# Kernel tuning notes

Measured on AMD Instinct MI355X. Metric: run time of the kernel, lower is better.

The kernel has to match this reference:

```python
import jax, jax.numpy as jnp
import numpy as np

B, S, H, C, T = 8, 1024, 256, 4, 12
THETA = 10000.0


def setup_inputs() -> dict:
    key = jax.random.key(0)
    ks = jax.random.split(key, 7)
    x = jax.random.normal(ks[0], (B, S, H), dtype=jnp.float32)
    token_index = jax.random.randint(ks[1], (B, S), 0, 256, dtype=jnp.int32)
    thread_id = jnp.sort(jax.random.randint(ks[2], (B, S), 0, T, dtype=jnp.int32), axis=-1)
    bound = 1.0 / np.sqrt(H)  # nn.Linear default init range
    Wq = jax.random.uniform(ks[3], (H, H * C), jnp.float32, -bound, bound)
    bq = jax.random.uniform(ks[4], (H * C,), jnp.float32, -bound, bound)
    Wk = jax.random.uniform(ks[5], (H, H * C), jnp.float32, -bound, bound)
    bk = jax.random.uniform(ks[6], (H * C,), jnp.float32, -bound, bound)
    return {"x": x, "Wq": Wq, "bq": bq, "Wk": Wk, "bk": bk,
            "token_index": token_index, "thread_id": thread_id}


def _rope(v, pos):
    # v: (B, S, C, H); pos: (B, S) signed positions
    half = v.shape[-1] // 2
    # freqs = 1 / theta^(arange(0, H, 2) / H)
    freqs = 1.0 / (THETA ** (jnp.arange(half, dtype=jnp.float32) * 2.0 / (2 * half)))
    ang = pos[..., None].astype(jnp.float32) * freqs          # (B, S, half)
    cos = jnp.cos(ang)[:, :, None, :]                          # (B, S, 1, half)
    sin = jnp.sin(ang)[:, :, None, :]
    vr = v.reshape(*v.shape[:-1], half, 2)                     # complex pairs (even, odd)
    re = vr[..., 0] * cos - vr[..., 1] * sin
    im = vr[..., 0] * sin + vr[..., 1] * cos
    return jnp.stack([re, im], axis=-1).reshape(v.shape)


def reference(x, Wq, bq, Wk, bk, token_index, thread_id):
    q = (x @ Wq + bq).reshape(B, S, C, H)
    k = (x @ Wk + bk).reshape(B, S, C, H)
    # Block sign rules of get_instance_embedding reduce to three cases per
    # token pair (m, n) with thread ids ti=thread(m), tj=thread(n):
    #   0 < ti < tj : q uses -pos, k uses +pos
    #   0 < tj < ti : q uses +pos, k uses -pos
    #   otherwise   : both use +pos
    q_pos = _rope(q, token_index)
    q_neg = _rope(q, -token_index)
    k_pos = _rope(k, token_index)
    k_neg = _rope(k, -token_index)
    l1 = jnp.einsum('bmch,bnch->bcmn', q_pos, k_pos)
    l2 = jnp.einsum('bmch,bnch->bcmn', q_neg, k_pos)
    l3 = jnp.einsum('bmch,bnch->bcmn', q_pos, k_neg)
    ti = thread_id[:, :, None]   # rows
    tj = thread_id[:, None, :]   # cols
    cond2 = ((ti > 0) & (ti < tj))[:, None, :, :]   # (B,1,S,S)
    cond3 = ((tj > 0) & (ti > tj))[:, None, :, :]
    return jnp.where(cond2, l2, jnp.where(cond3, l3, l1))  # (B, C, S, S)
```

## Files before the change

kernel.cpp:

```cpp
#include <hip/hip_runtime.h>

#define BB 8
#define SS 1024
#define HH 256
#define CC 4
#define NQ 1024

typedef unsigned short u16;
typedef unsigned int u32;
typedef __attribute__((ext_vector_type(8))) __bf16 bf16x8;
typedef __attribute__((ext_vector_type(4))) float f32x4;
typedef __attribute__((ext_vector_type(4))) u32 u32x4;
typedef __attribute__((ext_vector_type(4))) u16 u16x4;

__device__ __forceinline__ u16 f2bf(float f) {
    u32 u = __float_as_uint(f);
    u32 r = (u + 0x7FFFu + ((u >> 16) & 1u)) >> 16;
    return (u16)r;
}

__device__ __forceinline__ void gld16(const u16* g, u16* l) {
    __builtin_amdgcn_global_load_lds(
        (const __attribute__((address_space(1))) void*)g,
        (__attribute__((address_space(3))) void*)l, 16, 0, 0);
}

__device__ __forceinline__ bf16x8 ldsfrag(const u16* smem, int row, int c16) {
    const char* p = (const char*)smem + row * 128 + (((c16 ^ (row & 7)) & 7) << 4);
    return *(const bf16x8*)p;
}

__global__ void k0_castx(const float4* __restrict__ x, u16x4* __restrict__ xbf) {
    int i = blockIdx.x * 256 + threadIdx.x;
    float4 v = x[i];
    u16x4 o = {f2bf(v.x), f2bf(v.y), f2bf(v.z), f2bf(v.w)};
    xbf[i] = o;
}

__global__ void k0_transw(const float* __restrict__ Wq, const float* __restrict__ Wk,
                          u16* __restrict__ Wt) {
    __shared__ u16 tl[64][65];
    int nb = blockIdx.x * 64, kb = blockIdx.y * 64;
    int c = threadIdx.x & 63;
#pragma unroll
    for (int r = threadIdx.x >> 6; r < 64; r += 4) {
        int k = kb + r, n = nb + c;
        float v = (n < NQ) ? Wq[k * NQ + n] : Wk[k * NQ + (n - NQ)];
        tl[c][r] = f2bf(v);
    }
    __syncthreads();
#pragma unroll
    for (int r = threadIdx.x >> 6; r < 64; r += 4) {
        Wt[(size_t)(nb + r) * HH + kb + c] = tl[r][c];
    }
}

__global__ void k0_trig(float2* __restrict__ trig) {
    int i = blockIdx.x * 256 + threadIdx.x;
    int pos = i >> 7, f = i & 127;
    float freq = __expf(-(float)f * 0.07195578515529633f);
    float ang = (float)pos * freq;
    float s, c;
    sincosf(ang, &s, &c);
    trig[i] = make_float2(c, s);
}

#define STAGE_A(dst, srcbase, row0cnt4, m_off, kc)                                  \
    _Pragma("unroll") for (int i_ = 0; i_ < (row0cnt4); ++i_) {                     \
        int r_ = w * 8 * (row0cnt4) + i_ * 8 + (l >> 3);                            \
        int c16_ = (l & 7) ^ (r_ & 7);                                              \
        gld16((srcbase) + (size_t)((m_off) + r_) * HH + (kc) * 64 + c16_ * 8,       \
              (dst) + (w * 8 * (row0cnt4) + i_ * 8) * 64);                          \
    }

__global__ void __launch_bounds__(256) k1_proj(
    const u16* __restrict__ xbf, const u16* __restrict__ Wt,
    const float* __restrict__ bq, const float* __restrict__ bk,
    const int* __restrict__ tok, const float2* __restrict__ trig,
    u16* __restrict__ qpos, u16* __restrict__ qneg,
    u16* __restrict__ kpos, u16* __restrict__ kneg) {
    int wg = blockIdx.x;
    int m0 = (wg >> 5) * 128, n0 = (wg & 31) * 64;
    int w = threadIdx.x >> 6, l = threadIdx.x & 63;

    __shared__ u16 sm[24576];
    u16* Ab[2] = {sm, sm + 12288};
    u16* Bb[2] = {sm + 8192, sm + 20480};

    f32x4 acc[2][4] = {};
    STAGE_A(Ab[0], xbf, 4, m0, 0)
    STAGE_A(Bb[0], Wt, 2, n0, 0)
    asm volatile("s_waitcnt vmcnt(0)" ::: "memory");
    __builtin_amdgcn_s_barrier();
#pragma unroll
    for (int kc = 0; kc < 4; ++kc) {
        u16* As = Ab[kc & 1];
        u16* Bs = Bb[kc & 1];
        if (kc < 3) {
            STAGE_A(Ab[(kc + 1) & 1], xbf, 4, m0, kc + 1)
            STAGE_A(Bb[(kc + 1) & 1], Wt, 2, n0, kc + 1)
        }
#pragma unroll
        for (int ks = 0; ks < 2; ++ks) {
            int c16 = (l >> 4) + ks * 4;
            bf16x8 af[2], bfr[4];
#pragma unroll
            for (int mi = 0; mi < 2; ++mi) af[mi] = ldsfrag(As, w * 32 + mi * 16 + (l & 15), c16);
#pragma unroll
            for (int ns = 0; ns < 4; ++ns) bfr[ns] = ldsfrag(Bs, ns * 16 + (l & 15), c16);
#pragma unroll
            for (int mi = 0; mi < 2; ++mi)
#pragma unroll
                for (int ns = 0; ns < 4; ++ns)
                    acc[mi][ns] = __builtin_amdgcn_mfma_f32_16x16x32_bf16(af[mi], bfr[ns], acc[mi][ns], 0, 0, 0);
        }
        if (kc < 3) {
            asm volatile("s_waitcnt vmcnt(0) lgkmcnt(0)" ::: "memory");
            __builtin_amdgcn_s_barrier();
        }
    }

#pragma unroll
    for (int mi = 0; mi < 2; ++mi)
#pragma unroll
        for (int ns = 0; ns < 4; ++ns) {
            int n = n0 + ns * 16 + (l & 15);
            bool isq = n < NQ;
            int nc = n & (NQ - 1);
            float bias = isq ? bq[nc] : bk[nc];
            int c = nc >> 8, h = nc & 255, fi = h >> 1;
#pragma unroll
            for (int r = 0; r < 4; ++r) {
                int m = m0 + w * 32 + mi * 16 + (l >> 4) * 4 + r;
                float val = acc[mi][ns][r] + bias;
                float other = __shfl_xor(val, 1);
                int pos = tok[m];
                float2 cs = trig[pos * 128 + fi];
                float rp, rn;
                if ((l & 1) == 0) {
                    rp = val * cs.x - other * cs.y;
                    rn = val * cs.x + other * cs.y;
                } else {
                    rp = other * cs.y + val * cs.x;
                    rn = -other * cs.y + val * cs.x;
                }
                int b = m >> 10, s = m & 1023;
                size_t oidx = ((size_t)((b << 2) | c) * SS + s) * HH + h;
                if (isq) {
                    qpos[oidx] = f2bf(rp);
                    qneg[oidx] = f2bf(rn);
                } else {
                    kpos[oidx] = f2bf(rp);
                    kneg[oidx] = f2bf(rn);
                }
            }
        }
}

__global__ void __launch_bounds__(256) k2_gemm(
    const u16* __restrict__ qpos, const u16* __restrict__ qneg,
    const u16* __restrict__ kpos, const u16* __restrict__ kneg,
    const int* __restrict__ thread_id, float* __restrict__ out) {
    int wg = blockIdx.x;
    int bc = wg >> 7;
    int t = wg & 127;
    int m0 = (t >> 4) * 128, n0 = (t & 15) * 64;
    const int* tb = thread_id + (bc >> 2) * SS;
    int w = threadIdx.x >> 6, l = threadIdx.x & 63;
    int ti0 = tb[m0], ti1 = tb[m0 + 127], tj0 = tb[n0], tj1 = tb[n0 + 63];
    bool pure2 = (ti0 > 0) & (ti1 < tj0);
    bool pure3 = (tj0 > 0) & (ti0 > tj1);
    bool pure1 = (ti1 == 0) | (tj1 == 0) | ((ti0 == ti1) & (tj0 == tj1) & (ti0 == tj0));
    size_t base = (size_t)bc * (SS * HH);
    float* ob = out + (size_t)bc * ((size_t)SS * SS);
    int ar0 = m0 + w * 32;

    __shared__ u16 sm[24576];

    if (pure1 | pure2 | pure3) {
        const u16* q = (pure2 ? qneg : qpos) + base;
        const u16* k = (pure3 ? kneg : kpos) + base;
        u16* Ab[2] = {sm, sm + 12288};
        u16* Bb[2] = {sm + 8192, sm + 20480};

        f32x4 acc[2][4] = {};
        STAGE_A(Ab[0], q, 4, m0, 0)
        STAGE_A(Bb[0], k, 2, n0, 0)
        asm volatile("s_waitcnt vmcnt(0)" ::: "memory");
        __builtin_amdgcn_s_barrier();
#pragma unroll
        for (int kc = 0; kc < 4; ++kc) {
            u16* As = Ab[kc & 1];
            u16* Bs = Bb[kc & 1];
            if (kc < 3) {
                STAGE_A(Ab[(kc + 1) & 1], q, 4, m0, kc + 1)
                STAGE_A(Bb[(kc + 1) & 1], k, 2, n0, kc + 1)
            }
#pragma unroll
            for (int ks = 0; ks < 2; ++ks) {
                int c16 = (l >> 4) + ks * 4;
                bf16x8 af[2], bfr[4];
#pragma unroll
                for (int mi = 0; mi < 2; ++mi) af[mi] = ldsfrag(As, w * 32 + mi * 16 + (l & 15), c16);
#pragma unroll
                for (int ns = 0; ns < 4; ++ns) bfr[ns] = ldsfrag(Bs, ns * 16 + (l & 15), c16);
#pragma unroll
                for (int mi = 0; mi < 2; ++mi)
#pragma unroll
                    for (int ns = 0; ns < 4; ++ns)
                        acc[mi][ns] = __builtin_amdgcn_mfma_f32_16x16x32_bf16(af[mi], bfr[ns], acc[mi][ns], 0, 0, 0);
            }
            if (kc < 3) {
                asm volatile("s_waitcnt vmcnt(0) lgkmcnt(0)" ::: "memory");
                __builtin_amdgcn_s_barrier();
            }
        }

#pragma unroll
        for (int mi = 0; mi < 2; ++mi)
#pragma unroll
            for (int ns = 0; ns < 4; ++ns)
#pragma unroll
                for (int r = 0; r < 4; ++r) {
                    int m = ar0 + mi * 16 + (l >> 4) * 4 + r;
                    int n = n0 + ns * 16 + (l & 15);
                    ob[(size_t)m * SS + n] = acc[mi][ns][r];
                }
    } else {
        const u16* qp = qpos + base;
        const u16* qn = qneg + base;
        const u16* kp = kpos + base;
        const u16* kn = kneg + base;
        u16* smqp = sm;
        u16* smqn = sm + 8192;
        u16* smkp = sm + 16384;
        u16* smkn = sm + 20480;

        int bamin = ti0 > 1 ? ti0 : 1;
        int bcmin = tj0 > 1 ? tj0 : 1;
        bool B2 = (ti1 > 0) && (tj1 > bamin);
        bool B3 = (tj1 > 0) && (ti1 > bcmin);

        int fa[2], fb[2], fc[4], fd[4];
#pragma unroll
        for (int mi = 0; mi < 2; ++mi) {
            fa[mi] = tb[ar0 + mi * 16];
            fb[mi] = tb[ar0 + mi * 16 + 15];
        }
#pragma unroll
        for (int ns = 0; ns < 4; ++ns) {
            fc[ns] = tb[n0 + ns * 16];
            fd[ns] = tb[n0 + ns * 16 + 15];
        }
        u32 msk1 = 0, msk2 = 0, msk3 = 0;
#pragma unroll
        for (int mi = 0; mi < 2; ++mi)
#pragma unroll
            for (int ns = 0; ns < 4; ++ns) {
                u32 bit = 1u << (mi * 4 + ns);
                if ((fa[mi] == 0) | (fc[ns] == 0) | ((fa[mi] <= fd[ns]) & (fc[ns] <= fb[mi]))) msk1 |= bit;
                int amin = fa[mi] > 1 ? fa[mi] : 1;
                if ((fb[mi] > 0) & (fd[ns] > amin)) msk2 |= bit;
                int cmin = fc[ns] > 1 ? fc[ns] : 1;
                if ((fd[ns] > 0) & (fb[mi] > cmin)) msk3 |= bit;
            }
        msk1 = __builtin_amdgcn_readfirstlane(msk1);
        msk2 = __builtin_amdgcn_readfirstlane(msk2);
        msk3 = __builtin_amdgcn_readfirstlane(msk3);

        f32x4 a1[2][4] = {}, a2[2][4] = {}, a3[2][4] = {};
        for (int kc = 0; kc < 4; ++kc) {
            if (kc) __builtin_amdgcn_s_barrier();
            STAGE_A(smqp, qp, 4, m0, kc)
            if (B2) STAGE_A(smqn, qn, 4, m0, kc)
            STAGE_A(smkp, kp, 2, n0, kc)
            if (B3) STAGE_A(smkn, kn, 2, n0, kc)
            asm volatile("s_waitcnt vmcnt(0)" ::: "memory");
            __builtin_amdgcn_s_barrier();
#pragma unroll
            for (int ks = 0; ks < 2; ++ks) {
                int c16 = (l >> 4) + ks * 4;
                bf16x8 qpF[2], qnF[2], kpF[4], knF[4];
#pragma unroll
                for (int mi = 0; mi < 2; ++mi) {
                    int rr = w * 32 + mi * 16 + (l & 15);
                    qpF[mi] = ldsfrag(smqp, rr, c16);
                    if (msk2) qnF[mi] = ldsfrag(smqn, rr, c16);
                }
#pragma unroll
                for (int ns = 0; ns < 4; ++ns) {
                    int rn = ns * 16 + (l & 15);
                    kpF[ns] = ldsfrag(smkp, rn, c16);
                    if (msk3) knF[ns] = ldsfrag(smkn, rn, c16);
                }
#pragma unroll
                for (int mi = 0; mi < 2; ++mi)
#pragma unroll
                    for (int ns = 0; ns < 4; ++ns) {
                        u32 bit = 1u << (mi * 4 + ns);
                        if (msk1 & bit)
                            a1[mi][ns] = __builtin_amdgcn_mfma_f32_16x16x32_bf16(qpF[mi], kpF[ns], a1[mi][ns], 0, 0, 0);
                        if (msk2 & bit)
                            a2[mi][ns] = __builtin_amdgcn_mfma_f32_16x16x32_bf16(qnF[mi], kpF[ns], a2[mi][ns], 0, 0, 0);
                        if (msk3 & bit)
                            a3[mi][ns] = __builtin_amdgcn_mfma_f32_16x16x32_bf16(qpF[mi], knF[ns], a3[mi][ns], 0, 0, 0);
                    }
            }
        }

        int tj[4], ti_[2][4];
#pragma unroll
        for (int ns = 0; ns < 4; ++ns) tj[ns] = tb[n0 + ns * 16 + (l & 15)];
#pragma unroll
        for (int mi = 0; mi < 2; ++mi)
#pragma unroll
            for (int r = 0; r < 4; ++r) ti_[mi][r] = tb[ar0 + mi * 16 + (l >> 4) * 4 + r];

#pragma unroll
        for (int mi = 0; mi < 2; ++mi)
#pragma unroll
            for (int ns = 0; ns < 4; ++ns)
#pragma unroll
                for (int r = 0; r < 4; ++r) {
                    int m = ar0 + mi * 16 + (l >> 4) * 4 + r;
                    int n = n0 + ns * 16 + (l & 15);
                    int ti = ti_[mi][r], tjj = tj[ns];
                    float v = (ti > 0 && ti < tjj) ? a2[mi][ns][r]
                             : ((tjj > 0 && ti > tjj) ? a3[mi][ns][r] : a1[mi][ns][r]);
                    ob[(size_t)m * SS + n] = v;
                }
    }
}

extern "C" void kernel_launch(void* const* d_in, const int* in_sizes, int n_in,
                              void* d_out, int out_size, void* d_ws, size_t ws_size,
                              hipStream_t stream) {
    const float* x  = (const float*)d_in[0];
    const float* Wq = (const float*)d_in[1];
    const float* bq = (const float*)d_in[2];
    const float* Wk = (const float*)d_in[3];
    const float* bk = (const float*)d_in[4];
    const int* tok  = (const int*)d_in[5];
    const int* tid  = (const int*)d_in[6];
    float* out = (float*)d_out;

    char* ws = (char*)d_ws;
    const size_t MB = 1u << 20;
    u16* qpos = (u16*)(ws);
    u16* qneg = (u16*)(ws + 16 * MB);
    u16* kpos = (u16*)(ws + 32 * MB);
    u16* kneg = (u16*)(ws + 48 * MB);
    u16* xbf  = (u16*)(ws + 64 * MB);
    u16* Wt   = (u16*)(ws + 68 * MB);
    float2* trig = (float2*)(ws + 69 * MB);

    k0_castx<<<2048, 256, 0, stream>>>((const float4*)x, (u16x4*)xbf);
    dim3 tg(32, 4);
    k0_transw<<<tg, 256, 0, stream>>>(Wq, Wk, Wt);
    k0_trig<<<128, 256, 0, stream>>>(trig);
    k1_proj<<<2048, 256, 0, stream>>>(xbf, Wt, bq, bk, tok, trig, qpos, qneg, kpos, kneg);
    k2_gemm<<<4096, 256, 0, stream>>>(qpos, qneg, kpos, kneg, tid, out);
}
```

Baseline: 135.8 us.

## Enlarge GEMM tiles to 128x128 with 8 waves and XCD-aware block remap

```diff
diff --git a/kernel.cpp b/kernel.cpp
--- a/kernel.cpp
+++ b/kernel.cpp
@@ -65,31 +65,33 @@
     trig[i] = make_float2(c, s);
 }
 
-#define STAGE_A(dst, srcbase, row0cnt4, m_off, kc)                                  \
-    _Pragma("unroll") for (int i_ = 0; i_ < (row0cnt4); ++i_) {                     \
-        int r_ = w * 8 * (row0cnt4) + i_ * 8 + (l >> 3);                            \
-        int c16_ = (l & 7) ^ (r_ & 7);                                              \
-        gld16((srcbase) + (size_t)((m_off) + r_) * HH + (kc) * 64 + c16_ * 8,       \
-              (dst) + (w * 8 * (row0cnt4) + i_ * 8) * 64);                          \
-    }
-
-__global__ void __launch_bounds__(256) k1_proj(
+#define STAGE2(dst, srcbase, roff, kc)                                          \
+    _Pragma("unroll") for (int i_ = 0; i_ < 2; ++i_) {                          \
+        int r_ = ww * 16 + i_ * 8 + (l >> 3);                                   \
+        int c16_ = (l & 7) ^ (r_ & 7);                                          \
+        gld16((srcbase) + (size_t)((roff) + r_) * HH + (kc) * 64 + c16_ * 8,    \
+              (dst) + (ww * 16 + i_ * 8) * 64);                                 \
+    }
+
+__global__ void __launch_bounds__(512, 2) k1_proj(
     const u16* __restrict__ xbf, const u16* __restrict__ Wt,
     const float* __restrict__ bq, const float* __restrict__ bk,
     const int* __restrict__ tok, const float2* __restrict__ trig,
     u16* __restrict__ qpos, u16* __restrict__ qneg,
     u16* __restrict__ kpos, u16* __restrict__ kneg) {
-    int wg = blockIdx.x;
-    int m0 = (wg >> 5) * 128, n0 = (wg & 31) * 64;
-    int w = threadIdx.x >> 6, l = threadIdx.x & 63;
-
-    __shared__ u16 sm[24576];
-    u16* Ab[2] = {sm, sm + 12288};
-    u16* Bb[2] = {sm + 8192, sm + 20480};
+    int h = blockIdx.x;
+    int logical = (h & 7) * 128 + (h >> 3);
+    int m0 = (logical >> 4) * 128, n0 = (logical & 15) * 128;
+    int ww = threadIdx.x >> 6, l = threadIdx.x & 63;
+    int wr = ww >> 1, wc = ww & 1;
+
+    __shared__ u16 sm[32768];
+    u16* Ab[2] = {sm, sm + 16384};
+    u16* Bb[2] = {sm + 8192, sm + 24576};
 
     f32x4 acc[2][4] = {};
-    STAGE_A(Ab[0], xbf, 4, m0, 0)
-    STAGE_A(Bb[0], Wt, 2, n0, 0)
+    STAGE2(Ab[0], xbf, m0, 0)
+    STAGE2(Bb[0], Wt, n0, 0)
     asm volatile("s_waitcnt vmcnt(0)" ::: "memory");
     __builtin_amdgcn_s_barrier();
 #pragma unroll
@@ -97,17 +99,17 @@
         u16* As = Ab[kc & 1];
         u16* Bs = Bb[kc & 1];
         if (kc < 3) {
-            STAGE_A(Ab[(kc + 1) & 1], xbf, 4, m0, kc + 1)
-            STAGE_A(Bb[(kc + 1) & 1], Wt, 2, n0, kc + 1)
+            STAGE2(Ab[(kc + 1) & 1], xbf, m0, kc + 1)
+            STAGE2(Bb[(kc + 1) & 1], Wt, n0, kc + 1)
         }
 #pragma unroll
         for (int ks = 0; ks < 2; ++ks) {
             int c16 = (l >> 4) + ks * 4;
             bf16x8 af[2], bfr[4];
 #pragma unroll
-            for (int mi = 0; mi < 2; ++mi) af[mi] = ldsfrag(As, w * 32 + mi * 16 + (l & 15), c16);
-#pragma unroll
-            for (int ns = 0; ns < 4; ++ns) bfr[ns] = ldsfrag(Bs, ns * 16 + (l & 15), c16);
+            for (int mi = 0; mi < 2; ++mi) af[mi] = ldsfrag(As, wr * 32 + mi * 16 + (l & 15), c16);
+#pragma unroll
+            for (int ns = 0; ns < 4; ++ns) bfr[ns] = ldsfrag(Bs, wc * 64 + ns * 16 + (l & 15), c16);
 #pragma unroll
             for (int mi = 0; mi < 2; ++mi)
 #pragma unroll
@@ -124,14 +126,14 @@
     for (int mi = 0; mi < 2; ++mi)
 #pragma unroll
         for (int ns = 0; ns < 4; ++ns) {
-            int n = n0 + ns * 16 + (l & 15);
+            int n = n0 + wc * 64 + ns * 16 + (l & 15);
             bool isq = n < NQ;
             int nc = n & (NQ - 1);
             float bias = isq ? bq[nc] : bk[nc];
-            int c = nc >> 8, h = nc & 255, fi = h >> 1;
+            int c = nc >> 8, hh = nc & 255, fi = hh >> 1;
 #pragma unroll
             for (int r = 0; r < 4; ++r) {
-                int m = m0 + w * 32 + mi * 16 + (l >> 4) * 4 + r;
+                int m = m0 + wr * 32 + mi * 16 + (l >> 4) * 4 + r;
                 float val = acc[mi][ns][r] + bias;
                 float other = __shfl_xor(val, 1);
                 int pos = tok[m];
@@ -145,7 +147,7 @@
                     rn = -other * cs.y + val * cs.x;
                 }
                 int b = m >> 10, s = m & 1023;
-                size_t oidx = ((size_t)((b << 2) | c) * SS + s) * HH + h;
+                size_t oidx = ((size_t)((b << 2) | c) * SS + s) * HH + hh;
                 if (isq) {
                     qpos[oidx] = f2bf(rp);
                     qneg[oidx] = f2bf(rn);
@@ -157,35 +159,38 @@
         }
 }
 
-__global__ void __launch_bounds__(256) k2_gemm(
+__global__ void __launch_bounds__(512, 2) k2_gemm(
     const u16* __restrict__ qpos, const u16* __restrict__ qneg,
     const u16* __restrict__ kpos, const u16* __restrict__ kneg,
     const int* __restrict__ thread_id, float* __restrict__ out) {
-    int wg = blockIdx.x;
-    int bc = wg >> 7;
-    int t = wg & 127;
-    int m0 = (t >> 4) * 128, n0 = (t & 15) * 64;
+    int h = blockIdx.x;
+    int logical = (h & 7) * 256 + (h >> 3);
+    int bc = logical >> 6;
+    int t = logical & 63;
+    int m0 = (t >> 3) * 128, n0 = (t & 7) * 128;
     const int* tb = thread_id + (bc >> 2) * SS;
-    int w = threadIdx.x >> 6, l = threadIdx.x & 63;
-    int ti0 = tb[m0], ti1 = tb[m0 + 127], tj0 = tb[n0], tj1 = tb[n0 + 63];
+    int ww = threadIdx.x >> 6, l = threadIdx.x & 63;
+    int wr = ww >> 1, wc = ww & 1;
+    int ti0 = tb[m0], ti1 = tb[m0 + 127], tj0 = tb[n0], tj1 = tb[n0 + 127];
     bool pure2 = (ti0 > 0) & (ti1 < tj0);
     bool pure3 = (tj0 > 0) & (ti0 > tj1);
     bool pure1 = (ti1 == 0) | (tj1 == 0) | ((ti0 == ti1) & (tj0 == tj1) & (ti0 == tj0));
     size_t base = (size_t)bc * (SS * HH);
     float* ob = out + (size_t)bc * ((size_t)SS * SS);
-    int ar0 = m0 + w * 32;
-
-    __shared__ u16 sm[24576];
+    int ar0 = m0 + wr * 32;
+    int nb0 = n0 + wc * 64;
+
+    __shared__ u16 sm[32768];
 
     if (pure1 | pure2 | pure3) {
         const u16* q = (pure2 ? qneg : qpos) + base;
         const u16* k = (pure3 ? kneg : kpos) + base;
-        u16* Ab[2] = {sm, sm + 12288};
-        u16* Bb[2] = {sm + 8192, sm + 20480};
+        u16* Ab[2] = {sm, sm + 16384};
+        u16* Bb[2] = {sm + 8192, sm + 24576};
 
         f32x4 acc[2][4] = {};
-        STAGE_A(Ab[0], q, 4, m0, 0)
-        STAGE_A(Bb[0], k, 2, n0, 0)
+        STAGE2(Ab[0], q, m0, 0)
+        STAGE2(Bb[0], k, n0, 0)
         asm volatile("s_waitcnt vmcnt(0)" ::: "memory");
         __builtin_amdgcn_s_barrier();
 #pragma unroll
@@ -193,17 +198,17 @@
             u16* As = Ab[kc & 1];
             u16* Bs = Bb[kc & 1];
             if (kc < 3) {
-                STAGE_A(Ab[(kc + 1) & 1], q, 4, m0, kc + 1)
-                STAGE_A(Bb[(kc + 1) & 1], k, 2, n0, kc + 1)
+                STAGE2(Ab[(kc + 1) & 1], q, m0, kc + 1)
+                STAGE2(Bb[(kc + 1) & 1], k, n0, kc + 1)
             }
 #pragma unroll
             for (int ks = 0; ks < 2; ++ks) {
                 int c16 = (l >> 4) + ks * 4;
                 bf16x8 af[2], bfr[4];
 #pragma unroll
-                for (int mi = 0; mi < 2; ++mi) af[mi] = ldsfrag(As, w * 32 + mi * 16 + (l & 15), c16);
-#pragma unroll
-                for (int ns = 0; ns < 4; ++ns) bfr[ns] = ldsfrag(Bs, ns * 16 + (l & 15), c16);
+                for (int mi = 0; mi < 2; ++mi) af[mi] = ldsfrag(As, wr * 32 + mi * 16 + (l & 15), c16);
+#pragma unroll
+                for (int ns = 0; ns < 4; ++ns) bfr[ns] = ldsfrag(Bs, wc * 64 + ns * 16 + (l & 15), c16);
 #pragma unroll
                 for (int mi = 0; mi < 2; ++mi)
 #pragma unroll
@@ -223,7 +228,7 @@
 #pragma unroll
                 for (int r = 0; r < 4; ++r) {
                     int m = ar0 + mi * 16 + (l >> 4) * 4 + r;
-                    int n = n0 + ns * 16 + (l & 15);
+                    int n = nb0 + ns * 16 + (l & 15);
                     ob[(size_t)m * SS + n] = acc[mi][ns][r];
                 }
     } else {
@@ -234,7 +239,7 @@
         u16* smqp = sm;
         u16* smqn = sm + 8192;
         u16* smkp = sm + 16384;
-        u16* smkn = sm + 20480;
+        u16* smkn = sm + 24576;
 
         int bamin = ti0 > 1 ? ti0 : 1;
         int bcmin = tj0 > 1 ? tj0 : 1;
@@ -249,8 +254,8 @@
         }
 #pragma unroll
         for (int ns = 0; ns < 4; ++ns) {
-            fc[ns] = tb[n0 + ns * 16];
-            fd[ns] = tb[n0 + ns * 16 + 15];
+            fc[ns] = tb[nb0 + ns * 16];
+            fd[ns] = tb[nb0 + ns * 16 + 15];
         }
         u32 msk1 = 0, msk2 = 0, msk3 = 0;
 #pragma unroll
@@ -271,10 +276,10 @@
         f32x4 a1[2][4] = {}, a2[2][4] = {}, a3[2][4] = {};
         for (int kc = 0; kc < 4; ++kc) {
             if (kc) __builtin_amdgcn_s_barrier();
-            STAGE_A(smqp, qp, 4, m0, kc)
-            if (B2) STAGE_A(smqn, qn, 4, m0, kc)
-            STAGE_A(smkp, kp, 2, n0, kc)
-            if (B3) STAGE_A(smkn, kn, 2, n0, kc)
+            STAGE2(smqp, qp, m0, kc)
+            if (B2) STAGE2(smqn, qn, m0, kc)
+            STAGE2(smkp, kp, n0, kc)
+            if (B3) STAGE2(smkn, kn, n0, kc)
             asm volatile("s_waitcnt vmcnt(0)" ::: "memory");
             __builtin_amdgcn_s_barrier();
 #pragma unroll
@@ -283,13 +288,13 @@
                 bf16x8 qpF[2], qnF[2], kpF[4], knF[4];
 #pragma unroll
                 for (int mi = 0; mi < 2; ++mi) {
-                    int rr = w * 32 + mi * 16 + (l & 15);
+                    int rr = wr * 32 + mi * 16 + (l & 15);
                     qpF[mi] = ldsfrag(smqp, rr, c16);
                     if (msk2) qnF[mi] = ldsfrag(smqn, rr, c16);
                 }
 #pragma unroll
                 for (int ns = 0; ns < 4; ++ns) {
-                    int rn = ns * 16 + (l & 15);
+                    int rn = wc * 64 + ns * 16 + (l & 15);
                     kpF[ns] = ldsfrag(smkp, rn, c16);
                     if (msk3) knF[ns] = ldsfrag(smkn, rn, c16);
                 }
@@ -310,7 +315,7 @@
 
         int tj[4], ti_[2][4];
 #pragma unroll
-        for (int ns = 0; ns < 4; ++ns) tj[ns] = tb[n0 + ns * 16 + (l & 15)];
+        for (int ns = 0; ns < 4; ++ns) tj[ns] = tb[nb0 + ns * 16 + (l & 15)];
 #pragma unroll
         for (int mi = 0; mi < 2; ++mi)
 #pragma unroll
@@ -323,7 +328,7 @@
 #pragma unroll
                 for (int r = 0; r < 4; ++r) {
                     int m = ar0 + mi * 16 + (l >> 4) * 4 + r;
-                    int n = n0 + ns * 16 + (l & 15);
+                    int n = nb0 + ns * 16 + (l & 15);
                     int ti = ti_[mi][r], tjj = tj[ns];
                     float v = (ti > 0 && ti < tjj) ? a2[mi][ns][r]
                              : ((tjj > 0 && ti > tjj) ? a3[mi][ns][r] : a1[mi][ns][r]);
@@ -358,6 +363,6 @@
     dim3 tg(32, 4);
     k0_transw<<<tg, 256, 0, stream>>>(Wq, Wk, Wt);
     k0_trig<<<128, 256, 0, stream>>>(trig);
-    k1_proj<<<2048, 256, 0, stream>>>(xbf, Wt, bq, bk, tok, trig, qpos, qneg, kpos, kneg);
-    k2_gemm<<<4096, 256, 0, stream>>>(qpos, qneg, kpos, kneg, tid, out);
-}
+    k1_proj<<<1024, 512, 0, stream>>>(xbf, Wt, bq, bk, tok, trig, qpos, qneg, kpos, kneg);
+    k2_gemm<<<2048, 512, 0, stream>>>(qpos, qneg, kpos, kneg, tid, out);
+}
```

After: 123.5 us. -9.1%, faster.
